# Optimization experiments

Hardware: AMD Instinct MI355X
Metric: run time of the kernel (lower is better)

## Reference

```python
import jax, jax.numpy as jnp
import numpy as np

DIM = 512
LEVELS = 4
KSIZES = [3, 5, 7, 9]
NUM_HEADS = 4
GN_GROUPS = 4
GN_EPS = 1e-5
ROPE_BASE = 10000.0


def dwconv(x, w, b):
    # x: (B,C,H,W), w: (C,1,k,k) depthwise, b: (C,)
    y = jax.lax.conv_general_dilated(
        x, w, window_strides=(1, 1), padding='SAME',
        dimension_numbers=('NCHW', 'OIHW', 'NCHW'),
        feature_group_count=x.shape[1])
    return y + b[None, :, None, None]


def groupnorm(x, w, b):
    B, C, H, W = x.shape
    xg = x.reshape(B, GN_GROUPS, C // GN_GROUPS, H, W)
    mu = xg.mean(axis=(2, 3, 4), keepdims=True)
    var = xg.var(axis=(2, 3, 4), keepdims=True)
    xn = ((xg - mu) * jax.lax.rsqrt(var + GN_EPS)).reshape(B, C, H, W)
    return xn * w[None, :, None, None] + b[None, :, None, None]


def rope2d(x):
    # Faithful to the torch RoPE: rotations have shape (h, c//2) and broadcast
    # onto the trailing (w, c//2) dims of x (valid because h == w), so the
    # rotation angle effectively varies along the w axis.
    b, h, w, c = x.shape
    k_max = c // 2
    theta = 1.0 / (ROPE_BASE ** (jnp.arange(k_max, dtype=x.dtype) / k_max))
    angles = jnp.arange(h, dtype=x.dtype)[:, None] * theta[None, :]  # (h, k_max)
    cos = jnp.cos(angles)[None, None, :, :]  # broadcasts along w axis
    sin = jnp.sin(angles)[None, None, :, :]
    xp = x.reshape(b, h, w, k_max, 2)
    re, im = xp[..., 0], xp[..., 1]
    out_re = cos * re - sin * im
    out_im = cos * im + sin * re
    return jnp.stack([out_re, out_im], axis=-1).reshape(b, h, w, c)


def setup_inputs() -> dict:
    key = jax.random.key(0)
    ks = jax.random.split(key, 20)
    C = DIM
    inp = {'x': jax.random.normal(ks[0], (8, C, 64, 64), dtype=jnp.float32)}
    for i, k in enumerate(KSIZES):
        inp[f'conv_w{i}'] = jax.random.normal(ks[1 + i], (C, 1, k, k), dtype=jnp.float32) * 0.05
        inp[f'conv_b{i}'] = jnp.zeros((C,), dtype=jnp.float32)
        inp[f'gn_w{i}'] = jnp.ones((C,), dtype=jnp.float32)
        inp[f'gn_b{i}'] = jnp.zeros((C,), dtype=jnp.float32)
    inp['qk_w'] = jax.random.normal(ks[10], (2 * C, C), dtype=jnp.float32) * (C ** -0.5)
    inp['lepe_w'] = jax.random.normal(ks[11], (C, 1, 3, 3), dtype=jnp.float32) * 0.05
    inp['lepe_b'] = jnp.zeros((C,), dtype=jnp.float32)
    return inp


def reference(x, conv_w0, conv_b0, gn_w0, gn_b0, conv_w1, conv_b1, gn_w1, gn_b1,
              conv_w2, conv_b2, gn_w2, gn_b2, conv_w3, conv_b3, gn_w3, gn_b3,
              qk_w, lepe_w, lepe_b):
    conv_ws = [conv_w0, conv_w1, conv_w2, conv_w3]
    conv_bs = [conv_b0, conv_b1, conv_b2, conv_b3]
    gn_ws = [gn_w0, gn_w1, gn_w2, gn_w3]
    gn_bs = [gn_b0, gn_b1, gn_b2, gn_b3]

    # Multi-level depthwise conv -> GroupNorm -> sigmoid gate, averaged.
    fused = sum(jax.nn.sigmoid(groupnorm(dwconv(x, cw, cb), gw, gb))
                for cw, cb, gw, gb in zip(conv_ws, conv_bs, gn_ws, gn_bs)) / LEVELS

    b, c, h, w = fused.shape
    n = h * w
    H = NUM_HEADS
    hd = c // H

    tokens = fused.transpose(0, 2, 3, 1).reshape(b, n, c)  # (b, n, c)

    qk = tokens @ qk_w.T  # (b, n, 2c)
    q = jax.nn.elu(qk[..., :c]) + 1.0
    k = jax.nn.elu(qk[..., c:]) + 1.0
    v = tokens

    q_rope = rope2d(q.reshape(b, h, w, c)).reshape(b, n, H, hd).transpose(0, 2, 1, 3)
    k_rope = rope2d(k.reshape(b, h, w, c)).reshape(b, n, H, hd).transpose(0, 2, 1, 3)
    qh = q.reshape(b, n, H, hd).transpose(0, 2, 1, 3)  # (b,H,n,hd)
    kh = k.reshape(b, n, H, hd).transpose(0, 2, 1, 3)
    vh = v.reshape(b, n, H, hd).transpose(0, 2, 1, 3)

    k_mean = kh.mean(axis=2, keepdims=True)  # (b,H,1,hd)
    z = 1.0 / (jnp.einsum('bhnd,bhmd->bhnm', qh, k_mean) + 1e-6)  # (b,H,n,1)
    kv = jnp.einsum('bhnd,bhne->bhde', k_rope, vh) / n  # (b,H,hd,hd)
    attn = jnp.einsum('bhnd,bhde->bhne', q_rope, kv) * z  # (b,H,n,hd)

    out_tok = attn.transpose(0, 2, 1, 3).reshape(b, n, c)
    lepe_out = dwconv(fused, lepe_w, lepe_b)  # (b,c,h,w)
    out_tok = out_tok + lepe_out.transpose(0, 2, 3, 1).reshape(b, n, c)

    return out_tok.transpose(0, 2, 1).reshape(b, c, h, w)
```

## Files before the change

### kernel.cpp

```cpp
#include <hip/hip_runtime.h>
#include <math.h>


typedef __attribute__((ext_vector_type(8))) short bf8;
typedef __attribute__((ext_vector_type(4))) float f32x4;

__device__ __forceinline__ float waveSum(float v) {
  #pragma unroll
  for (int o = 32; o; o >>= 1) v += __shfl_down(v, o, 64);
  return v;
}

__device__ __forceinline__ unsigned short f2bf(float f) {
  unsigned u = __float_as_uint(f);
  unsigned r = u + 0x7fffu + ((u >> 16) & 1u);
  return (unsigned short)(r >> 16);
}

__device__ __forceinline__ float bf2f(unsigned short u) {
  return __uint_as_float((unsigned)u << 16);
}

__device__ __forceinline__ void gload_lds16(const void* g, void* l) {
  __builtin_amdgcn_global_load_lds(
      (const __attribute__((address_space(1))) unsigned*)g,
      (__attribute__((address_space(3))) unsigned*)l, 16, 0, 0);
}

__global__ __launch_bounds__(256) void k_ropetab(float* __restrict__ tab) {
  int idx = blockIdx.x * 256 + threadIdx.x;
  int w = idx >> 8, kk = idx & 255;
  float theta = powf(10000.0f, -(float)kk * (1.0f / 256.0f));
  float ang = (float)w * theta;
  tab[2 * idx]     = cosf(ang);
  tab[2 * idx + 1] = sinf(ang);
}

template <int K>
__device__ __forceinline__ void conv8(float (*sm)[73], const float* wl,
                                      int r, int cb, float bias, float acc[8]) {
  constexpr int P = (K - 1) / 2;
  #pragma unroll
  for (int i = 0; i < 8; i++) acc[i] = bias;
  #pragma unroll
  for (int dy = 0; dy < K; ++dy) {
    const float* row = &sm[r + dy - P + 4][cb - P + 4];
    float v[8 + K - 1];
    #pragma unroll
    for (int o = 0; o < 8 + K - 1; ++o) v[o] = row[o];
    #pragma unroll
    for (int dx = 0; dx < K; ++dx) {
      float wv = wl[dy * K + dx];
      #pragma unroll
      for (int i = 0; i < 8; i++) acc[i] = fmaf(wv, v[i + dx], acc[i]);
    }
  }
}

__device__ __forceinline__ void load_plane512(const float* __restrict__ xp,
                                              float (*sm)[73], int tid) {
  for (int idx = tid; idx < 5184; idx += 512) {
    int pr = idx / 72, pc = idx - pr * 72;
    int gr = pr - 4, gc = pc - 4;
    float v = 0.f;
    if ((unsigned)gr < 64u && (unsigned)gc < 64u) v = xp[gr * 64 + gc];
    sm[pr][pc] = v;
  }
}

__device__ __forceinline__ void load_weights512(const float* w0, const float* w1,
                                                const float* w2, const float* w3,
                                                float* wl, int c, int tid) {
  if (tid < 9)               wl[tid] = w0[c * 9  + tid];
  else if (tid < 34)         wl[tid] = w1[c * 25 + tid - 9];
  else if (tid < 83)         wl[tid] = w2[c * 49 + tid - 34];
  else if (tid < 164)        wl[tid] = w3[c * 81 + tid - 83];
}

__device__ __forceinline__ void reduce_write2_512(float s, float sq, float* red,
                                                  int tid, float* dst) {
  s = waveSum(s); sq = waveSum(sq);
  int wid = tid >> 6, lane = tid & 63;
  if (lane == 0) { red[wid] = s; red[8 + wid] = sq; }
  __syncthreads();
  if (tid == 0) {
    float S = 0.f, SQ = 0.f;
    #pragma unroll
    for (int i = 0; i < 8; i++) { S += red[i]; SQ += red[8 + i]; }
    dst[0] = S; dst[1] = SQ;
  }
  __syncthreads();
}

__global__ __launch_bounds__(512) void k_conv4(
    const float* __restrict__ x,
    const float* __restrict__ w0, const float* __restrict__ b0,
    const float* __restrict__ w1, const float* __restrict__ b1,
    const float* __restrict__ w2, const float* __restrict__ b2,
    const float* __restrict__ w3, const float* __restrict__ b3,
    float* __restrict__ part,
    unsigned short* __restrict__ l0, unsigned short* __restrict__ l1,
    unsigned short* __restrict__ l2, unsigned short* __restrict__ l3) {
  __shared__ float sm[72][73];
  __shared__ float wl[164];
  __shared__ float red[16];
  int tid = threadIdx.x;
  int bc = blockIdx.x;
  int b = bc >> 9, c = bc & 511;
  load_plane512(x + (size_t)bc * 4096, sm, tid);
  load_weights512(w0, w1, w2, w3, wl, c, tid);
  __syncthreads();
  int r = tid >> 3, cb = (tid & 7) << 3;
  size_t obase = (size_t)bc * 4096 + r * 64 + cb;
  float acc[8];
  float s, sq;
  unsigned short o[8];

  conv8<3>(sm, &wl[0], r, cb, b0[c], acc);
  s = 0; sq = 0;
  #pragma unroll
  for (int i = 0; i < 8; i++) {
    s += acc[i]; sq = fmaf(acc[i], acc[i], sq); o[i] = f2bf(acc[i]);
  }
  *(uint4*)&l0[obase] = *(uint4*)&o[0];
  reduce_write2_512(s, sq, red, tid, part + ((size_t)(0 * 8 + b) * 512 + c) * 2);
  __builtin_amdgcn_sched_barrier(0);

  conv8<5>(sm, &wl[9], r, cb, b1[c], acc);
  s = 0; sq = 0;
  #pragma unroll
  for (int i = 0; i < 8; i++) {
    s += acc[i]; sq = fmaf(acc[i], acc[i], sq); o[i] = f2bf(acc[i]);
  }
  *(uint4*)&l1[obase] = *(uint4*)&o[0];
  reduce_write2_512(s, sq, red, tid, part + ((size_t)(1 * 8 + b) * 512 + c) * 2);
  __builtin_amdgcn_sched_barrier(0);

  conv8<7>(sm, &wl[34], r, cb, b2[c], acc);
  s = 0; sq = 0;
  #pragma unroll
  for (int i = 0; i < 8; i++) {
    s += acc[i]; sq = fmaf(acc[i], acc[i], sq); o[i] = f2bf(acc[i]);
  }
  *(uint4*)&l2[obase] = *(uint4*)&o[0];
  reduce_write2_512(s, sq, red, tid, part + ((size_t)(2 * 8 + b) * 512 + c) * 2);
  __builtin_amdgcn_sched_barrier(0);

  conv8<9>(sm, &wl[83], r, cb, b3[c], acc);
  s = 0; sq = 0;
  #pragma unroll
  for (int i = 0; i < 8; i++) {
    s += acc[i]; sq = fmaf(acc[i], acc[i], sq); o[i] = f2bf(acc[i]);
  }
  *(uint4*)&l3[obase] = *(uint4*)&o[0];
  reduce_write2_512(s, sq, red, tid, part + ((size_t)(3 * 8 + b) * 512 + c) * 2);
}

__global__ __launch_bounds__(128) void k_gn_stats(const float* __restrict__ part,
                                                  float* __restrict__ stats) {
  int blk = blockIdx.x;
  int tid = threadIdx.x;
  int g = blk & 3, bb = (blk >> 2) & 7, l = blk >> 5;
  const float* p = part + ((size_t)(l * 8 + bb) * 512 + g * 128 + tid) * 2;
  float s = p[0], sq = p[1];
  s = waveSum(s); sq = waveSum(sq);
  __shared__ float red[4];
  int wid = tid >> 6, lane = tid & 63;
  if (lane == 0) { red[wid] = s; red[2 + wid] = sq; }
  __syncthreads();
  if (tid == 0) {
    float S = red[0] + red[1], SQ = red[2] + red[3];
    const float inv = 1.0f / (128.0f * 4096.0f);
    float mean = S * inv;
    float var = SQ * inv - mean * mean;
    stats[blk * 2] = mean;
    stats[blk * 2 + 1] = rsqrtf(var + 1e-5f);
  }
}

__global__ __launch_bounds__(256) void k_fused_tp(
    const unsigned short* __restrict__ l0, const unsigned short* __restrict__ l1,
    const unsigned short* __restrict__ l2, const unsigned short* __restrict__ l3,
    const float* __restrict__ gw0, const float* __restrict__ gb0,
    const float* __restrict__ gw1, const float* __restrict__ gb1,
    const float* __restrict__ gw2, const float* __restrict__ gb2,
    const float* __restrict__ gw3, const float* __restrict__ gb3,
    const float* __restrict__ stats, unsigned short* __restrict__ fnchw,
    unsigned short* __restrict__ fbf) {
  __shared__ float smT[64][65];
  int tid = threadIdx.x;
  int bid = blockIdx.x;
  int nt = bid & 63, ct = (bid >> 6) & 7, b = bid >> 9;
  int c0 = ct << 6, n0 = nt << 6;
  int c_loc = tid >> 2, nq = tid & 3;
  int c = c0 + c_loc, g = c >> 7;
  float m0 = stats[(0 * 32 + b * 4 + g) * 2], r0 = stats[(0 * 32 + b * 4 + g) * 2 + 1];
  float m1 = stats[(1 * 32 + b * 4 + g) * 2], r1 = stats[(1 * 32 + b * 4 + g) * 2 + 1];
  float m2 = stats[(2 * 32 + b * 4 + g) * 2], r2 = stats[(2 * 32 + b * 4 + g) * 2 + 1];
  float m3 = stats[(3 * 32 + b * 4 + g) * 2], r3 = stats[(3 * 32 + b * 4 + g) * 2 + 1];
  float a0 = r0 * gw0[c], c0p = gb0[c] - m0 * a0;
  float a1 = r1 * gw1[c], c1p = gb1[c] - m1 * a1;
  float a2 = r2 * gw2[c], c2p = gb2[c] - m2 * a2;
  float a3 = r3 * gw3[c], c3p = gb3[c] - m3 * a3;
  size_t base = ((size_t)b * 512 + c) * 4096 + n0 + nq * 16;
  uint4 u0a = *(const uint4*)&l0[base], u0b = *(const uint4*)&l0[base + 8];
  uint4 u1a = *(const uint4*)&l1[base], u1b = *(const uint4*)&l1[base + 8];
  uint4 u2a = *(const uint4*)&l2[base], u2b = *(const uint4*)&l2[base + 8];
  uint4 u3a = *(const uint4*)&l3[base], u3b = *(const uint4*)&l3[base + 8];
  float outv[16];
  #pragma unroll
  for (int i = 0; i < 8; i++) {
    float t0 = fmaf(bf2f(((const unsigned short*)&u0a)[i]), a0, c0p);
    float t1 = fmaf(bf2f(((const unsigned short*)&u1a)[i]), a1, c1p);
    float t2 = fmaf(bf2f(((const unsigned short*)&u2a)[i]), a2, c2p);
    float t3 = fmaf(bf2f(((const unsigned short*)&u3a)[i]), a3, c3p);
    float s = 1.0f / (1.0f + __expf(-t0)) + 1.0f / (1.0f + __expf(-t1)) +
              1.0f / (1.0f + __expf(-t2)) + 1.0f / (1.0f + __expf(-t3));
    outv[i] = s * 0.25f;
  }
  #pragma unroll
  for (int i = 0; i < 8; i++) {
    float t0 = fmaf(bf2f(((const unsigned short*)&u0b)[i]), a0, c0p);
    float t1 = fmaf(bf2f(((const unsigned short*)&u1b)[i]), a1, c1p);
    float t2 = fmaf(bf2f(((const unsigned short*)&u2b)[i]), a2, c2p);
    float t3 = fmaf(bf2f(((const unsigned short*)&u3b)[i]), a3, c3p);
    float s = 1.0f / (1.0f + __expf(-t0)) + 1.0f / (1.0f + __expf(-t1)) +
              1.0f / (1.0f + __expf(-t2)) + 1.0f / (1.0f + __expf(-t3));
    outv[8 + i] = s * 0.25f;
  }
  unsigned short ob[16];
  #pragma unroll
  for (int i = 0; i < 16; i++) ob[i] = f2bf(outv[i]);
  *(uint4*)&fnchw[base]     = *(uint4*)&ob[0];
  *(uint4*)&fnchw[base + 8] = *(uint4*)&ob[8];
  #pragma unroll
  for (int i = 0; i < 16; i++) smT[c_loc][nq * 16 + i] = outv[i];
  __syncthreads();
  int cc = tid & 63, r_s = tid >> 6;
  #pragma unroll
  for (int rr = 0; rr < 64; rr += 4)
    fbf[((size_t)b * 4096 + n0 + rr + r_s) * 512 + c0 + cc] = f2bf(smT[cc][rr + r_s]);
}

__global__ __launch_bounds__(256) void k_wcvt(const float* __restrict__ qkw,
                                              unsigned short* __restrict__ wbf) {
  int gid = blockIdx.x * 256 + threadIdx.x;
  float4 v = *(const float4*)&qkw[(size_t)gid * 4];
  short4 o;
  o.x = (short)f2bf(v.x); o.y = (short)f2bf(v.y);
  o.z = (short)f2bf(v.z); o.w = (short)f2bf(v.w);
  *(short4*)&wbf[(size_t)gid * 4] = o;
}

__global__ __launch_bounds__(256) void k_qk(const unsigned short* __restrict__ fbf,
                                            const unsigned short* __restrict__ wbf,
                                            float* __restrict__ qbuf,
                                            float* __restrict__ kbuf) {
  __shared__ __align__(16) short As[8192];
  __shared__ __align__(16) short Bs[8192];
  int tid = threadIdx.x;
  int bid = blockIdx.x;
  int sw = (bid & 7) * 256 + (bid >> 3);
  int b = sw >> 8, rem = sw & 255;
  int mt_blk = rem >> 3, jt = rem & 7;
  int m0 = mt_blk << 7, j0 = jt << 7;
  int lane = tid & 63, wid = tid >> 6;
  int wm = (wid >> 1) * 64, wn = (wid & 1) * 64;
  int l15 = lane & 15, l4 = lane >> 4;

  const unsigned short* Ab = fbf + (size_t)b * 4096 * 512;
  f32x4 acc[4][4];
  #pragma unroll
  for (int i = 0; i < 4; i++)
    #pragma unroll
    for (int j = 0; j < 4; j++) acc[i][j] = (f32x4)0.f;

  int srow[4], sperm[4];
  #pragma unroll
  for (int i = 0; i < 4; i++) {
    int s = i * 256 + tid;
    srow[i] = s >> 3;
    sperm[i] = (s & 7) ^ (srow[i] & 7);
  }

  for (int t = 0; t < 8; ++t) {
    int c0 = t << 6;
    if (t) __syncthreads();
    #pragma unroll
    for (int i = 0; i < 4; i++) {
      int s = i * 256 + tid;
      gload_lds16(Ab + (size_t)(m0 + srow[i]) * 512 + c0 + sperm[i] * 8,
                  (char*)As + s * 16);
      gload_lds16(wbf + (size_t)(j0 + srow[i]) * 512 + c0 + sperm[i] * 8,
                  (char*)Bs + s * 16);
    }
    __syncthreads();
    #pragma unroll
    for (int ks = 0; ks < 2; ++ks) {
      bf8 af[4], bfr[4];
      #pragma unroll
      for (int mt = 0; mt < 4; mt++) {
        int row = wm + mt * 16 + l15;
        int g = ks * 4 + l4;
        af[mt] = *(const bf8*)((const char*)As + row * 128 + ((g ^ (row & 7)) << 4));
      }
      #pragma unroll
      for (int nt = 0; nt < 4; nt++) {
        int row = wn + nt * 16 + l15;
        int g = ks * 4 + l4;
        bfr[nt] = *(const bf8*)((const char*)Bs + row * 128 + ((g ^ (row & 7)) << 4));
      }
      #pragma unroll
      for (int mt = 0; mt < 4; mt++)
        #pragma unroll
        for (int nt = 0; nt < 4; nt++)
          acc[mt][nt] = __builtin_amdgcn_mfma_f32_16x16x32_bf16(
              af[mt], bfr[nt], acc[mt][nt], 0, 0, 0);
    }
  }

  float* dst; int jb;
  if (j0 < 512) { dst = qbuf; jb = j0; } else { dst = kbuf; jb = j0 - 512; }
  #pragma unroll
  for (int mt = 0; mt < 4; mt++) {
    #pragma unroll
    for (int nt = 0; nt < 4; nt++) {
      #pragma unroll
      for (int r = 0; r < 4; r++) {
        float v = acc[mt][nt][r];
        v = v > 0.f ? v + 1.f : __expf(v);
        int token = m0 + wm + mt * 16 + l4 * 4 + r;
        int chan = jb + wn + nt * 16 + l15;
        dst[((size_t)b * 4096 + token) * 512 + chan] = v;
      }
    }
  }
}

__global__ __launch_bounds__(256) void k_krT(const float* __restrict__ kbuf,
                                             const float* __restrict__ tab,
                                             unsigned short* __restrict__ krT,
                                             float* __restrict__ kmp) {
  __shared__ float sm[64][65];
  int tid = threadIdx.x;
  int bid = blockIdx.x;
  int nt = bid & 63, ct = (bid >> 6) & 7, b = bid >> 9;
  int c0 = ct << 6, n0 = nt << 6;
  int cc = tid & 63, n_s = tid >> 6;
  #pragma unroll
  for (int nn = 0; nn < 64; nn += 4)
    sm[cc][nn + n_s] = kbuf[((size_t)b * 4096 + n0 + nn + n_s) * 512 + c0 + cc];
  __syncthreads();
  int rc = tid >> 2, nq = tid & 3;
  int c = c0 + rc;
  int pairidx = c >> 1;
  int odd = c & 1;
  int partner = odd ? rc - 1 : rc + 1;
  unsigned short o[16];
  float colsum = 0.f;
  #pragma unroll
  for (int i = 0; i < 16; i++) {
    int nloc = nq * 16 + i;
    float2 cs = *(const float2*)&tab[2 * (nloc * 256 + pairidx)];
    float a = sm[rc][nloc], p = sm[partner][nloc];
    float r = odd ? fmaf(cs.x, a, cs.y * p) : fmaf(cs.x, a, -cs.y * p);
    o[i] = f2bf(r);
    colsum += a;
  }
  *(uint4*)&krT[((size_t)b * 512 + c) * 4096 + n0 + nq * 16]     = *(uint4*)&o[0];
  *(uint4*)&krT[((size_t)b * 512 + c) * 4096 + n0 + nq * 16 + 8] = *(uint4*)&o[8];
  colsum += __shfl_xor(colsum, 1, 64);
  colsum += __shfl_xor(colsum, 2, 64);
  if (nq == 0) kmp[((size_t)b * 64 + nt) * 512 + c] = colsum;
}

__global__ __launch_bounds__(512) void k_kmean_fin(const float* __restrict__ kmp,
                                                   float* __restrict__ kmean) {
  int b = blockIdx.x, c = threadIdx.x;
  float s = 0.f;
  for (int nt = 0; nt < 64; nt++) s += kmp[((size_t)b * 64 + nt) * 512 + c];
  kmean[b * 512 + c] = s * (1.0f / 4096.0f);
}

__global__ __launch_bounds__(256) void k_zrope(const float* __restrict__ qbuf,
                                               const float* __restrict__ kmean,
                                               const float* __restrict__ tab,
                                               float* __restrict__ zbuf,
                                               unsigned short* __restrict__ qr) {
  __shared__ float kml[512];
  int tid = threadIdx.x;
  int blk = blockIdx.x;
  int b = blk >> 10;
  kml[tid] = kmean[b * 512 + tid];
  kml[tid + 256] = kmean[b * 512 + 256 + tid];
  __syncthreads();
  int tok = blk * 4 + (tid >> 6);
  int pg = tid & 63;
  int n = tok & 4095;
  int wpos = n & 63;
  const float* qp = qbuf + (size_t)tok * 512 + pg * 8;
  const float* tp = tab + 2 * (wpos * 256 + pg * 4);
  float4 a  = *(const float4*)&qp[0];
  float4 b4 = *(const float4*)&qp[4];
  float4 t0 = *(const float4*)&tp[0];
  float4 t1 = *(const float4*)&tp[4];
  unsigned short o[8];
  o[0] = f2bf(t0.x * a.x - t0.y * a.y);
  o[1] = f2bf(t0.x * a.y + t0.y * a.x);
  o[2] = f2bf(t0.z * a.z - t0.w * a.w);
  o[3] = f2bf(t0.z * a.w + t0.w * a.z);
  o[4] = f2bf(t1.x * b4.x - t1.y * b4.y);
  o[5] = f2bf(t1.x * b4.y + t1.y * b4.x);
  o[6] = f2bf(t1.z * b4.z - t1.w * b4.w);
  o[7] = f2bf(t1.z * b4.w + t1.w * b4.z);
  *(uint4*)&qr[(size_t)tok * 512 + pg * 8] = *(uint4*)o;
  const float* km = &kml[pg * 8];
  float4 ka = *(const float4*)&km[0];
  float4 kb = *(const float4*)&km[4];
  float dot = a.x * ka.x + a.y * ka.y + a.z * ka.z + a.w * ka.w +
              b4.x * kb.x + b4.y * kb.y + b4.z * kb.z + b4.w * kb.w;
  dot += __shfl_xor(dot, 1, 64);
  dot += __shfl_xor(dot, 2, 64);
  dot += __shfl_xor(dot, 4, 64);
  dot += __shfl_xor(dot, 8, 64);
  if ((pg & 15) == 0) {
    int h = pg >> 4;
    zbuf[(size_t)(b * 4 + h) * 4096 + n] = 1.0f / (dot + 1e-6f);
  }
}

__global__ __launch_bounds__(256) void k_kv(const unsigned short* __restrict__ krT,
                                            const unsigned short* __restrict__ fnchw,
                                            float* __restrict__ kvpart) {
  __shared__ __align__(16) short As[8192];
  __shared__ __align__(16) short Bs[8192];
  int tid = threadIdx.x;
  int bid = blockIdx.x;
  int bh = bid >> 3, chunk = bid & 7;
  int b = bh >> 2, h = bh & 3;
  int n_base = chunk * 512;
  int lane = tid & 63, wid = tid >> 6;
  int wm = (wid >> 1) * 64, wn = (wid & 1) * 64;
  int l15 = lane & 15, l4 = lane >> 4;

  const unsigned short* Ab = krT + ((size_t)b * 512 + h * 128) * 4096;
  const unsigned short* Vb = fnchw + ((size_t)b * 512 + h * 128) * 4096;
  f32x4 acc[4][4];
  #pragma unroll
  for (int i = 0; i < 4; i++)
    #pragma unroll
    for (int j = 0; j < 4; j++) acc[i][j] = (f32x4)0.f;

  int srow[4], sperm[4];
  #pragma unroll
  for (int i = 0; i < 4; i++) {
    int s = i * 256 + tid;
    srow[i] = s >> 3;
    sperm[i] = (s & 7) ^ (srow[i] & 7);
  }

  for (int t = 0; t < 8; ++t) {
    int k0 = n_base + (t << 6);
    if (t) __syncthreads();
    #pragma unroll
    for (int i = 0; i < 4; i++) {
      int s = i * 256 + tid;
      gload_lds16(Ab + (size_t)srow[i] * 4096 + k0 + sperm[i] * 8,
                  (char*)As + s * 16);
      gload_lds16(Vb + (size_t)srow[i] * 4096 + k0 + sperm[i] * 8,
                  (char*)Bs + s * 16);
    }
    __syncthreads();
    #pragma unroll
    for (int ks = 0; ks < 2; ++ks) {
      bf8 af[4], bfr[4];
      #pragma unroll
      for (int mt = 0; mt < 4; mt++) {
        int row = wm + mt * 16 + l15;
        int g = ks * 4 + l4;
        af[mt] = *(const bf8*)((const char*)As + row * 128 + ((g ^ (row & 7)) << 4));
      }
      #pragma unroll
      for (int nt = 0; nt < 4; nt++) {
        int row = wn + nt * 16 + l15;
        int g = ks * 4 + l4;
        bfr[nt] = *(const bf8*)((const char*)Bs + row * 128 + ((g ^ (row & 7)) << 4));
      }
      #pragma unroll
      for (int mt = 0; mt < 4; mt++)
        #pragma unroll
        for (int nt = 0; nt < 4; nt++)
          acc[mt][nt] = __builtin_amdgcn_mfma_f32_16x16x32_bf16(
              af[mt], bfr[nt], acc[mt][nt], 0, 0, 0);
    }
  }

  float* dst = kvpart + (size_t)(bh * 8 + chunk) * 16384;
  #pragma unroll
  for (int mt = 0; mt < 4; mt++) {
    #pragma unroll
    for (int nt = 0; nt < 4; nt++) {
      #pragma unroll
      for (int r = 0; r < 4; r++) {
        int d = wm + mt * 16 + l4 * 4 + r;
        int e = wn + nt * 16 + l15;
        dst[d * 128 + e] = acc[mt][nt][r];
      }
    }
  }
}

__global__ __launch_bounds__(256) void k_kv_fin(const float* __restrict__ part,
                                                unsigned short* __restrict__ kvT) {
  int bh = blockIdx.x;
  int tid = threadIdx.x;
  for (int idx = tid; idx < 16384; idx += 256) {
    int e = idx >> 7, d = idx & 127;
    float s = 0;
    for (int ch = 0; ch < 8; ch++)
      s += part[(size_t)(bh * 8 + ch) * 16384 + d * 128 + e];
    kvT[(size_t)bh * 16384 + idx] = f2bf(s * (1.0f / 4096.0f));
  }
}

__global__ __launch_bounds__(256) void k_lepe(const unsigned short* __restrict__ fnchw,
                                              const float* __restrict__ lw,
                                              const float* __restrict__ lb,
                                              float* __restrict__ out) {
  __shared__ float sm[66][67];
  __shared__ float wl[9];
  int tid = threadIdx.x;
  int bc = blockIdx.x;
  int c = bc & 511;
  const unsigned short* fp = fnchw + (size_t)bc * 4096;
  for (int idx = tid; idx < 4356; idx += 256) {
    int pr = idx / 66, pc = idx - pr * 66;
    int gr = pr - 1, gc = pc - 1;
    float v = 0.f;
    if ((unsigned)gr < 64u && (unsigned)gc < 64u) v = bf2f(fp[gr * 64 + gc]);
    sm[pr][pc] = v;
  }
  if (tid < 9) wl[tid] = lw[c * 9 + tid];
  __syncthreads();
  int r = tid >> 2, cb = (tid & 3) << 4;
  float bias = lb[c];
  float accv[16];
  #pragma unroll
  for (int i = 0; i < 16; i++) accv[i] = bias;
  #pragma unroll
  for (int dy = 0; dy < 3; dy++) {
    const float* row = &sm[r + dy][cb];
    float v[18];
    #pragma unroll
    for (int o = 0; o < 18; ++o) v[o] = row[o];
    #pragma unroll
    for (int dx = 0; dx < 3; dx++) {
      float wv = wl[dy * 3 + dx];
      #pragma unroll
      for (int i = 0; i < 16; i++) accv[i] = fmaf(wv, v[i + dx], accv[i]);
    }
  }
  float* op = out + (size_t)bc * 4096 + r * 64 + cb;
  #pragma unroll
  for (int i = 0; i < 16; i += 4)
    *(float4*)&op[i] = make_float4(accv[i], accv[i + 1], accv[i + 2], accv[i + 3]);
}

__global__ __launch_bounds__(256) void k_attn(const unsigned short* __restrict__ qr,
                                              const unsigned short* __restrict__ kvT,
                                              const float* __restrict__ zbuf,
                                              float* __restrict__ out) {
  __shared__ __align__(16) short As[8192];
  __shared__ __align__(16) short Bs[8192];
  __shared__ float zl[128];
  int tid = threadIdx.x;
  int bid = blockIdx.x;
  int sw = (bid & 7) * 128 + (bid >> 3);
  int b = sw >> 7, rem = sw & 127;
  int h = rem >> 5, mt_blk = rem & 31;
  int bh = b * 4 + h;
  int m0 = mt_blk << 7;
  int lane = tid & 63, wid = tid >> 6;
  int wm = (wid >> 1) * 64, wn = (wid & 1) * 64;
  int l15 = lane & 15, l4 = lane >> 4;

  const unsigned short* Ab = qr + (size_t)b * 4096 * 512 + h * 128;
  const unsigned short* Bb = kvT + (size_t)bh * 16384;
  if (tid < 128) zl[tid] = zbuf[(size_t)bh * 4096 + m0 + tid];

  f32x4 acc[4][4];
  #pragma unroll
  for (int i = 0; i < 4; i++)
    #pragma unroll
    for (int j = 0; j < 4; j++) acc[i][j] = (f32x4)0.f;

  int srow[4], sperm[4];
  #pragma unroll
  for (int i = 0; i < 4; i++) {
    int s = i * 256 + tid;
    srow[i] = s >> 3;
    sperm[i] = (s & 7) ^ (srow[i] & 7);
  }

  for (int t = 0; t < 2; ++t) {
    int c0 = t << 6;
    if (t) __syncthreads();
    #pragma unroll
    for (int i = 0; i < 4; i++) {
      int s = i * 256 + tid;
      gload_lds16(Ab + (size_t)(m0 + srow[i]) * 512 + c0 + sperm[i] * 8,
                  (char*)As + s * 16);
      gload_lds16(Bb + srow[i] * 128 + c0 + sperm[i] * 8,
                  (char*)Bs + s * 16);
    }
    __syncthreads();
    #pragma unroll
    for (int ks = 0; ks < 2; ++ks) {
      bf8 af[4], bfr[4];
      #pragma unroll
      for (int mt = 0; mt < 4; mt++) {
        int row = wm + mt * 16 + l15;
        int g = ks * 4 + l4;
        af[mt] = *(const bf8*)((const char*)As + row * 128 + ((g ^ (row & 7)) << 4));
      }
      #pragma unroll
      for (int nt = 0; nt < 4; nt++) {
        int row = wn + nt * 16 + l15;
        int g = ks * 4 + l4;
        bfr[nt] = *(const bf8*)((const char*)Bs + row * 128 + ((g ^ (row & 7)) << 4));
      }
      #pragma unroll
      for (int mt = 0; mt < 4; mt++)
        #pragma unroll
        for (int nt = 0; nt < 4; nt++)
          acc[mt][nt] = __builtin_amdgcn_mfma_f32_16x16x32_bf16(
              af[mt], bfr[nt], acc[mt][nt], 0, 0, 0);
    }
  }

  #pragma unroll
  for (int mt = 0; mt < 4; mt++) {
    int tl = wm + mt * 16 + l4 * 4;
    float4 zv = make_float4(zl[tl], zl[tl + 1], zl[tl + 2], zl[tl + 3]);
    #pragma unroll
    for (int nt = 0; nt < 4; nt++) {
      int e = wn + nt * 16 + l15;
      float* op = &out[((size_t)b * 512 + h * 128 + e) * 4096 + m0 + tl];
      float4 o4 = *(float4*)op;
      o4.x += acc[mt][nt][0] * zv.x;
      o4.y += acc[mt][nt][1] * zv.y;
      o4.z += acc[mt][nt][2] * zv.z;
      o4.w += acc[mt][nt][3] * zv.w;
      *(float4*)op = o4;
    }
  }
}

extern "C" void kernel_launch(void* const* d_in, const int* in_sizes, int n_in,
                              void* d_out, int out_size, void* d_ws, size_t ws_size,
                              hipStream_t stream) {
  (void)in_sizes; (void)n_in; (void)out_size; (void)ws_size;
  const float* x   = (const float*)d_in[0];
  const float* cw0 = (const float*)d_in[1];
  const float* cb0 = (const float*)d_in[2];
  const float* gw0 = (const float*)d_in[3];
  const float* gb0 = (const float*)d_in[4];
  const float* cw1 = (const float*)d_in[5];
  const float* cb1 = (const float*)d_in[6];
  const float* gw1 = (const float*)d_in[7];
  const float* gb1 = (const float*)d_in[8];
  const float* cw2 = (const float*)d_in[9];
  const float* cb2 = (const float*)d_in[10];
  const float* gw2 = (const float*)d_in[11];
  const float* gb2 = (const float*)d_in[12];
  const float* cw3 = (const float*)d_in[13];
  const float* cb3 = (const float*)d_in[14];
  const float* gw3 = (const float*)d_in[15];
  const float* gb3 = (const float*)d_in[16];
  const float* qkw = (const float*)d_in[17];
  const float* lw  = (const float*)d_in[18];
  const float* lb  = (const float*)d_in[19];
  float* out = (float*)d_out;
  float* ws  = (float*)d_ws;

  float* fslot    = ws;
  float* qbuf     = fslot + 16777216;
  float* convpart = qbuf + 16777216;
  float* gnstats  = convpart + 32768;
  float* tab      = gnstats + 256;
  float* kmp      = tab + 32768;
  float* kmean    = kmp + 262144;
  float* zbuf     = kmean + 4096;
  float* wslot    = zbuf + 131072;
  float* regionR  = wslot + 262144;
  float* kvpart   = regionR + 8388608;
  float* kbuf     = out;
  unsigned short* lvl0    = (unsigned short*)qbuf;
  unsigned short* lvl1    = (unsigned short*)kvpart;
  unsigned short* lvl2    = (unsigned short*)out;
  unsigned short* lvl3    = (unsigned short*)out + 16777216;
  unsigned short* fnchw   = (unsigned short*)fslot;
  unsigned short* qropebf = (unsigned short*)fslot + 16777216;
  unsigned short* fbf     = (unsigned short*)regionR;
  unsigned short* krT     = (unsigned short*)regionR;
  unsigned short* wbf     = (unsigned short*)wslot;
  unsigned short* kvT     = (unsigned short*)wslot;

  k_ropetab<<<dim3(64), dim3(256), 0, stream>>>(tab);
  k_conv4<<<dim3(4096), dim3(512), 0, stream>>>(
      x, cw0, cb0, cw1, cb1, cw2, cb2, cw3, cb3, convpart,
      lvl0, lvl1, lvl2, lvl3);
  k_gn_stats<<<dim3(128), dim3(128), 0, stream>>>(convpart, gnstats);
  k_fused_tp<<<dim3(4096), dim3(256), 0, stream>>>(
      lvl0, lvl1, lvl2, lvl3,
      gw0, gb0, gw1, gb1, gw2, gb2, gw3, gb3, gnstats, fnchw, fbf);
  k_wcvt<<<dim3(512), dim3(256), 0, stream>>>(qkw, wbf);
  k_qk<<<dim3(2048), dim3(256), 0, stream>>>(fbf, wbf, qbuf, kbuf);
  k_krT<<<dim3(4096), dim3(256), 0, stream>>>(kbuf, tab, krT, kmp);
  k_kmean_fin<<<dim3(8), dim3(512), 0, stream>>>(kmp, kmean);
  k_kv<<<dim3(256), dim3(256), 0, stream>>>(krT, fnchw, kvpart);
  k_kv_fin<<<dim3(32), dim3(256), 0, stream>>>(kvpart, kvT);
  k_lepe<<<dim3(4096), dim3(256), 0, stream>>>(fnchw, lw, lb, out);
  k_zrope<<<dim3(8192), dim3(256), 0, stream>>>(qbuf, kmean, tab, zbuf, qropebf);
  k_attn<<<dim3(1024), dim3(256), 0, stream>>>(qropebf, kvT, zbuf, out);
}
```

Measured before the change: 483.7 us.

## Pair conv levels sharing LDS row loads and store q/k as bf16

```diff
diff --git a/kernel.cpp b/kernel.cpp
--- a/kernel.cpp
+++ b/kernel.cpp
@@ -34,27 +34,6 @@
   float ang = (float)w * theta;
   tab[2 * idx]     = cosf(ang);
   tab[2 * idx + 1] = sinf(ang);
-}
-
-template <int K>
-__device__ __forceinline__ void conv8(float (*sm)[73], const float* wl,
-                                      int r, int cb, float bias, float acc[8]) {
-  constexpr int P = (K - 1) / 2;
-  #pragma unroll
-  for (int i = 0; i < 8; i++) acc[i] = bias;
-  #pragma unroll
-  for (int dy = 0; dy < K; ++dy) {
-    const float* row = &sm[r + dy - P + 4][cb - P + 4];
-    float v[8 + K - 1];
-    #pragma unroll
-    for (int o = 0; o < 8 + K - 1; ++o) v[o] = row[o];
-    #pragma unroll
-    for (int dx = 0; dx < K; ++dx) {
-      float wv = wl[dy * K + dx];
-      #pragma unroll
-      for (int i = 0; i < 8; i++) acc[i] = fmaf(wv, v[i + dx], acc[i]);
-    }
-  }
 }
 
 __device__ __forceinline__ void load_plane512(const float* __restrict__ xp,
@@ -90,6 +69,19 @@
     dst[0] = S; dst[1] = SQ;
   }
   __syncthreads();
+}
+
+__device__ __forceinline__ void store_level(float acc[8], size_t obase,
+                                            unsigned short* dst, float* red,
+                                            int tid, float* pdst) {
+  float s = 0.f, sq = 0.f;
+  unsigned short o[8];
+  #pragma unroll
+  for (int i = 0; i < 8; i++) {
+    s += acc[i]; sq = fmaf(acc[i], acc[i], sq); o[i] = f2bf(acc[i]);
+  }
+  *(uint4*)&dst[obase] = *(uint4*)&o[0];
+  reduce_write2_512(s, sq, red, tid, pdst);
 }
 
 __global__ __launch_bounds__(512) void k_conv4(
@@ -112,48 +104,71 @@
   __syncthreads();
   int r = tid >> 3, cb = (tid & 7) << 3;
   size_t obase = (size_t)bc * 4096 + r * 64 + cb;
-  float acc[8];
-  float s, sq;
-  unsigned short o[8];
-
-  conv8<3>(sm, &wl[0], r, cb, b0[c], acc);
-  s = 0; sq = 0;
-  #pragma unroll
-  for (int i = 0; i < 8; i++) {
-    s += acc[i]; sq = fmaf(acc[i], acc[i], sq); o[i] = f2bf(acc[i]);
-  }
-  *(uint4*)&l0[obase] = *(uint4*)&o[0];
-  reduce_write2_512(s, sq, red, tid, part + ((size_t)(0 * 8 + b) * 512 + c) * 2);
+
+  {
+    float a0[8], a1[8];
+    float bi0 = b0[c], bi1 = b1[c];
+    #pragma unroll
+    for (int i = 0; i < 8; i++) { a0[i] = bi0; a1[i] = bi1; }
+    #pragma unroll
+    for (int dy = -2; dy <= 2; ++dy) {
+      const float* row = &sm[r + dy + 4][cb + 2];
+      float v[12];
+      #pragma unroll
+      for (int o = 0; o < 12; ++o) v[o] = row[o];
+      #pragma unroll
+      for (int dx = 0; dx < 5; ++dx) {
+        float wv = wl[9 + (dy + 2) * 5 + dx];
+        #pragma unroll
+        for (int i = 0; i < 8; i++) a1[i] = fmaf(wv, v[i + dx], a1[i]);
+      }
+      if (dy >= -1 && dy <= 1) {
+        #pragma unroll
+        for (int dx = 0; dx < 3; ++dx) {
+          float wv = wl[(dy + 1) * 3 + dx];
+          #pragma unroll
+          for (int i = 0; i < 8; i++) a0[i] = fmaf(wv, v[i + dx + 1], a0[i]);
+        }
+      }
+    }
+    store_level(a0, obase, l0, red, tid,
+                part + ((size_t)(0 * 8 + b) * 512 + c) * 2);
+    store_level(a1, obase, l1, red, tid,
+                part + ((size_t)(1 * 8 + b) * 512 + c) * 2);
+  }
   __builtin_amdgcn_sched_barrier(0);
 
-  conv8<5>(sm, &wl[9], r, cb, b1[c], acc);
-  s = 0; sq = 0;
-  #pragma unroll
-  for (int i = 0; i < 8; i++) {
-    s += acc[i]; sq = fmaf(acc[i], acc[i], sq); o[i] = f2bf(acc[i]);
-  }
-  *(uint4*)&l1[obase] = *(uint4*)&o[0];
-  reduce_write2_512(s, sq, red, tid, part + ((size_t)(1 * 8 + b) * 512 + c) * 2);
-  __builtin_amdgcn_sched_barrier(0);
-
-  conv8<7>(sm, &wl[34], r, cb, b2[c], acc);
-  s = 0; sq = 0;
-  #pragma unroll
-  for (int i = 0; i < 8; i++) {
-    s += acc[i]; sq = fmaf(acc[i], acc[i], sq); o[i] = f2bf(acc[i]);
-  }
-  *(uint4*)&l2[obase] = *(uint4*)&o[0];
-  reduce_write2_512(s, sq, red, tid, part + ((size_t)(2 * 8 + b) * 512 + c) * 2);
-  __builtin_amdgcn_sched_barrier(0);
-
-  conv8<9>(sm, &wl[83], r, cb, b3[c], acc);
-  s = 0; sq = 0;
-  #pragma unroll
-  for (int i = 0; i < 8; i++) {
-    s += acc[i]; sq = fmaf(acc[i], acc[i], sq); o[i] = f2bf(acc[i]);
-  }
-  *(uint4*)&l3[obase] = *(uint4*)&o[0];
-  reduce_write2_512(s, sq, red, tid, part + ((size_t)(3 * 8 + b) * 512 + c) * 2);
+  {
+    float a2[8], a3[8];
+    float bi2 = b2[c], bi3 = b3[c];
+    #pragma unroll
+    for (int i = 0; i < 8; i++) { a2[i] = bi2; a3[i] = bi3; }
+    #pragma unroll
+    for (int dy = -4; dy <= 4; ++dy) {
+      const float* row = &sm[r + dy + 4][cb];
+      float v[16];
+      #pragma unroll
+      for (int o = 0; o < 16; ++o) v[o] = row[o];
+      #pragma unroll
+      for (int dx = 0; dx < 9; ++dx) {
+        float wv = wl[83 + (dy + 4) * 9 + dx];
+        #pragma unroll
+        for (int i = 0; i < 8; i++) a3[i] = fmaf(wv, v[i + dx], a3[i]);
+      }
+      if (dy >= -3 && dy <= 3) {
+        #pragma unroll
+        for (int dx = 0; dx < 7; ++dx) {
+          float wv = wl[34 + (dy + 3) * 7 + dx];
+          #pragma unroll
+          for (int i = 0; i < 8; i++) a2[i] = fmaf(wv, v[i + dx + 1], a2[i]);
+        }
+      }
+    }
+    store_level(a2, obase, l2, red, tid,
+                part + ((size_t)(2 * 8 + b) * 512 + c) * 2);
+    store_level(a3, obase, l3, red, tid,
+                part + ((size_t)(3 * 8 + b) * 512 + c) * 2);
+  }
 }
 
 __global__ __launch_bounds__(128) void k_gn_stats(const float* __restrict__ part,
@@ -254,8 +269,8 @@
 
 __global__ __launch_bounds__(256) void k_qk(const unsigned short* __restrict__ fbf,
                                             const unsigned short* __restrict__ wbf,
-                                            float* __restrict__ qbuf,
-                                            float* __restrict__ kbuf) {
+                                            unsigned short* __restrict__ qbf,
+                                            unsigned short* __restrict__ kbf) {
   __shared__ __align__(16) short As[8192];
   __shared__ __align__(16) short Bs[8192];
   int tid = threadIdx.x;
@@ -319,8 +334,8 @@
     }
   }
 
-  float* dst; int jb;
-  if (j0 < 512) { dst = qbuf; jb = j0; } else { dst = kbuf; jb = j0 - 512; }
+  unsigned short* dst; int jb;
+  if (j0 < 512) { dst = qbf; jb = j0; } else { dst = kbf; jb = j0 - 512; }
   #pragma unroll
   for (int mt = 0; mt < 4; mt++) {
     #pragma unroll
@@ -331,13 +346,13 @@
         v = v > 0.f ? v + 1.f : __expf(v);
         int token = m0 + wm + mt * 16 + l4 * 4 + r;
         int chan = jb + wn + nt * 16 + l15;
-        dst[((size_t)b * 4096 + token) * 512 + chan] = v;
-      }
-    }
-  }
-}
-
-__global__ __launch_bounds__(256) void k_krT(const float* __restrict__ kbuf,
+        dst[((size_t)b * 4096 + token) * 512 + chan] = f2bf(v);
+      }
+    }
+  }
+}
+
+__global__ __launch_bounds__(256) void k_krT(const unsigned short* __restrict__ kbf,
                                              const float* __restrict__ tab,
                                              unsigned short* __restrict__ krT,
                                              float* __restrict__ kmp) {
@@ -349,7 +364,8 @@
   int cc = tid & 63, n_s = tid >> 6;
   #pragma unroll
   for (int nn = 0; nn < 64; nn += 4)
-    sm[cc][nn + n_s] = kbuf[((size_t)b * 4096 + n0 + nn + n_s) * 512 + c0 + cc];
+    sm[cc][nn + n_s] =
+        bf2f(kbf[((size_t)b * 4096 + n0 + nn + n_s) * 512 + c0 + cc]);
   __syncthreads();
   int rc = tid >> 2, nq = tid & 3;
   int c = c0 + rc;
@@ -382,7 +398,7 @@
   kmean[b * 512 + c] = s * (1.0f / 4096.0f);
 }
 
-__global__ __launch_bounds__(256) void k_zrope(const float* __restrict__ qbuf,
+__global__ __launch_bounds__(256) void k_zrope(const unsigned short* __restrict__ qbf,
                                                const float* __restrict__ kmean,
                                                const float* __restrict__ tab,
                                                float* __restrict__ zbuf,
@@ -398,10 +414,11 @@
   int pg = tid & 63;
   int n = tok & 4095;
   int wpos = n & 63;
-  const float* qp = qbuf + (size_t)tok * 512 + pg * 8;
+  uint4 qu = *(const uint4*)&qbf[(size_t)tok * 512 + pg * 8];
+  const unsigned short* qs = (const unsigned short*)&qu;
+  float4 a  = make_float4(bf2f(qs[0]), bf2f(qs[1]), bf2f(qs[2]), bf2f(qs[3]));
+  float4 b4 = make_float4(bf2f(qs[4]), bf2f(qs[5]), bf2f(qs[6]), bf2f(qs[7]));
   const float* tp = tab + 2 * (wpos * 256 + pg * 4);
-  float4 a  = *(const float4*)&qp[0];
-  float4 b4 = *(const float4*)&qp[4];
   float4 t0 = *(const float4*)&tp[0];
   float4 t1 = *(const float4*)&tp[4];
   unsigned short o[8];
@@ -684,8 +701,8 @@
   float* ws  = (float*)d_ws;
 
   float* fslot    = ws;
-  float* qbuf     = fslot + 16777216;
-  float* convpart = qbuf + 16777216;
+  float* qslot    = fslot + 16777216;
+  float* convpart = qslot + 16777216;
   float* gnstats  = convpart + 32768;
   float* tab      = gnstats + 256;
   float* kmp      = tab + 32768;
@@ -694,13 +711,14 @@
   float* wslot    = zbuf + 131072;
   float* regionR  = wslot + 262144;
   float* kvpart   = regionR + 8388608;
-  float* kbuf     = out;
-  unsigned short* lvl0    = (unsigned short*)qbuf;
+  unsigned short* lvl0    = (unsigned short*)qslot;
   unsigned short* lvl1    = (unsigned short*)kvpart;
   unsigned short* lvl2    = (unsigned short*)out;
   unsigned short* lvl3    = (unsigned short*)out + 16777216;
   unsigned short* fnchw   = (unsigned short*)fslot;
   unsigned short* qropebf = (unsigned short*)fslot + 16777216;
+  unsigned short* qbf     = (unsigned short*)qslot;
+  unsigned short* kbf     = (unsigned short*)out;
   unsigned short* fbf     = (unsigned short*)regionR;
   unsigned short* krT     = (unsigned short*)regionR;
   unsigned short* wbf     = (unsigned short*)wslot;
@@ -715,12 +733,12 @@
       lvl0, lvl1, lvl2, lvl3,
       gw0, gb0, gw1, gb1, gw2, gb2, gw3, gb3, gnstats, fnchw, fbf);
   k_wcvt<<<dim3(512), dim3(256), 0, stream>>>(qkw, wbf);
-  k_qk<<<dim3(2048), dim3(256), 0, stream>>>(fbf, wbf, qbuf, kbuf);
-  k_krT<<<dim3(4096), dim3(256), 0, stream>>>(kbuf, tab, krT, kmp);
+  k_qk<<<dim3(2048), dim3(256), 0, stream>>>(fbf, wbf, qbf, kbf);
+  k_krT<<<dim3(4096), dim3(256), 0, stream>>>(kbf, tab, krT, kmp);
   k_kmean_fin<<<dim3(8), dim3(512), 0, stream>>>(kmp, kmean);
   k_kv<<<dim3(256), dim3(256), 0, stream>>>(krT, fnchw, kvpart);
   k_kv_fin<<<dim3(32), dim3(256), 0, stream>>>(kvpart, kvT);
   k_lepe<<<dim3(4096), dim3(256), 0, stream>>>(fnchw, lw, lb, out);
-  k_zrope<<<dim3(8192), dim3(256), 0, stream>>>(qbuf, kmean, tab, zbuf, qropebf);
+  k_zrope<<<dim3(8192), dim3(256), 0, stream>>>(qbf, kmean, tab, zbuf, qropebf);
   k_attn<<<dim3(1024), dim3(256), 0, stream>>>(qropebf, kvT, zbuf, out);
 }
```

After: 894.5 us. +84.9%, slower.
